# Performance work log

Hardware: AMD Instinct MI355X
Metric: run time of the kernel (lower is better)

The kernel has to match this reference:

```python
import jax, jax.numpy as jnp
import numpy as np

HEADS = 16
DIM_HEAD = 64
EPS = 1e-5


def _layernorm(x, w, b):
    mu = jnp.mean(x, axis=-1, keepdims=True)
    var = jnp.var(x, axis=-1, keepdims=True)
    return (x - mu) * jax.lax.rsqrt(var + EPS) * w + b


def setup_inputs() -> dict:
    key = jax.random.key(0)
    ks = jax.random.split(key, 6)
    B, F, Q, D = 8, 4096, 64, 1024
    inner = HEADS * DIM_HEAD  # 1024
    s = 0.02
    return {
        "features": jax.random.normal(ks[0], (B, F, D), jnp.float32),
        "latents": jax.random.normal(ks[1], (B, Q, D), jnp.float32),
        "lnm_w": jnp.ones((D,), jnp.float32),
        "lnm_b": jnp.zeros((D,), jnp.float32),
        "lnl_w": jnp.ones((D,), jnp.float32),
        "lnl_b": jnp.zeros((D,), jnp.float32),
        "Wq": jax.random.normal(ks[2], (D, inner), jnp.float32) * s,
        "Wk": jax.random.normal(ks[3], (D, inner), jnp.float32) * s,
        "Wv": jax.random.normal(ks[4], (D, inner), jnp.float32) * s,
        "Wo": jax.random.normal(ks[5], (inner, D), jnp.float32) * s,
    }


def reference(features, latents, lnm_w, lnm_b, lnl_w, lnl_b, Wq, Wk, Wv, Wo):
    B, Q = latents.shape[0], latents.shape[1]
    scale = DIM_HEAD ** (-0.5)

    x = _layernorm(features, lnm_w, lnm_b)           # (B, F, D)
    lat = _layernorm(latents, lnl_w, lnl_b)          # (B, Q, D)

    q = (lat @ Wq).reshape(B, Q, HEADS, DIM_HEAD).transpose(0, 2, 1, 3)  # b h q d
    kv_in = jnp.concatenate([x, lat], axis=1)        # (B, F+Q, D)
    FL = kv_in.shape[1]
    k = (kv_in @ Wk).reshape(B, FL, HEADS, DIM_HEAD).transpose(0, 2, 1, 3)  # b h f d
    v = (kv_in @ Wv).reshape(B, FL, HEADS, DIM_HEAD).transpose(0, 2, 1, 3)  # b h f d

    sim = jnp.einsum('bhqd,bhfd->bhqf', q * scale, k)
    alphas = jax.nn.softmax(sim, axis=-1)            # amax-subtract is folded into stable softmax
    out = jnp.einsum('bhqf,bhfv->bhqv', alphas, v)
    out = out.transpose(0, 2, 1, 3).reshape(B, Q, HEADS * DIM_HEAD)
    return out @ Wo
```

## Files before the change

### kernel.cpp

```cpp
#include <hip/hip_runtime.h>


typedef float   f32x4  __attribute__((ext_vector_type(4)));
typedef short   bf16x8 __attribute__((ext_vector_type(8)));

#define MFMA_BF16 __builtin_amdgcn_mfma_f32_16x16x32_bf16

__device__ __forceinline__ unsigned short f2bf(float f) {
  unsigned u = __float_as_uint(f);
  unsigned r = (u + 0x7fffu + ((u >> 16) & 1u)) >> 16;
  return (unsigned short)r;
}

__device__ __forceinline__ void gload_lds16(const unsigned short* g, unsigned short* l) {
  __builtin_amdgcn_global_load_lds(
      (const __attribute__((address_space(1))) unsigned int*)g,
      (__attribute__((address_space(3))) unsigned int*)l, 16, 0, 0);
}

__global__ __launch_bounds__(256) void ln_kernel(
    const float* __restrict__ features, const float* __restrict__ latents,
    const float* __restrict__ lnm_w, const float* __restrict__ lnm_b,
    const float* __restrict__ lnl_w, const float* __restrict__ lnl_b,
    unsigned short* __restrict__ kv_ln, unsigned short* __restrict__ lat_ln)
{
  const int row = blockIdx.x;
  const int b  = row / 4160;
  const int fi = row - b * 4160;
  const bool is_lat = fi >= 4096;
  const float* x = is_lat ? (latents + (size_t)(b * 64 + fi - 4096) * 1024)
                          : (features + (size_t)(b * 4096 + fi) * 1024);
  const float* wp = is_lat ? lnl_w : lnm_w;
  const float* bp = is_lat ? lnl_b : lnm_b;
  const int tid = threadIdx.x;

  float4 v = *(const float4*)(x + tid * 4);
  float s  = v.x + v.y + v.z + v.w;
  float s2 = v.x * v.x + v.y * v.y + v.z * v.z + v.w * v.w;
#pragma unroll
  for (int sh = 1; sh < 64; sh <<= 1) {
    s  += __shfl_xor(s,  sh, 64);
    s2 += __shfl_xor(s2, sh, 64);
  }
  __shared__ float red[8];
  if ((tid & 63) == 0) { red[tid >> 6] = s; red[4 + (tid >> 6)] = s2; }
  __syncthreads();
  s  = red[0] + red[1] + red[2] + red[3];
  s2 = red[4] + red[5] + red[6] + red[7];
  const float mu   = s * (1.0f / 1024.0f);
  const float var  = s2 * (1.0f / 1024.0f) - mu * mu;
  const float rstd = rsqrtf(var + 1e-5f);

  float4 w4 = *(const float4*)(wp + tid * 4);
  float4 b4 = *(const float4*)(bp + tid * 4);
  ushort4 o;
  o.x = f2bf((v.x - mu) * rstd * w4.x + b4.x);
  o.y = f2bf((v.y - mu) * rstd * w4.y + b4.y);
  o.z = f2bf((v.z - mu) * rstd * w4.z + b4.z);
  o.w = f2bf((v.w - mu) * rstd * w4.w + b4.w);
  *(ushort4*)(kv_ln + (size_t)row * 1024 + tid * 4) = o;
  if (is_lat)
    *(ushort4*)(lat_ln + (size_t)(b * 64 + fi - 4096) * 1024 + tid * 4) = o;
}

__global__ __launch_bounds__(256) void wcast_kernel(
    const float* __restrict__ Wq, const float* __restrict__ Wk,
    const float* __restrict__ Wv, const float* __restrict__ Wo,
    unsigned short* __restrict__ Wkv_t, unsigned short* __restrict__ Wq_t,
    unsigned short* __restrict__ Wo_t)
{
  __shared__ float tile[32][33];
  const int kt = blockIdx.x * 32, nt = blockIdx.y * 32;
  const int tx = threadIdx.x & 31, ty = threadIdx.x >> 5;

  const float* src; int nc; float scale = 1.0f;
  if (nt < 1024)      { src = Wk; nc = nt; }
  else if (nt < 2048) { src = Wv; nc = nt - 1024; }
  else if (nt < 3072) { src = Wq; nc = nt - 2048; scale = 0.125f; }
  else                { src = Wo; nc = nt - 3072; }

#pragma unroll
  for (int kk = 0; kk < 4; ++kk)
    tile[ty + kk * 8][tx] = src[(size_t)(kt + ty + kk * 8) * 1024 + nc + tx] * scale;
  __syncthreads();

#pragma unroll
  for (int nn = 0; nn < 4; ++nn) {
    const int ng = nt + ty + nn * 8;
    unsigned short* d;
    if (ng < 2048)      d = Wkv_t + (size_t)ng * 1024;
    else if (ng < 3072) d = Wq_t + (size_t)(ng - 2048) * 1024;
    else                d = Wo_t + (size_t)(ng - 3072) * 1024;
    d[kt + tx] = f2bf(tile[tx][ty + nn * 8]);
  }
}

__global__ __launch_bounds__(512, 4) void gemm256_bf16(
    const unsigned short* __restrict__ A,
    const unsigned short* __restrict__ Bt,
    unsigned short* __restrict__ Kp, unsigned short* __restrict__ Vp,
    int M, int N, int K)
{
  __shared__ __align__(16) unsigned short lds[36864];
  const int tid  = threadIdx.x;
  const int wave = tid >> 6, lane = tid & 63;
  const int lo = lane & 15, hi = lane >> 4;
  const int wr = wave >> 1, wc = wave & 1;

  const int nbn = gridDim.x;
  int flat = blockIdx.y * nbn + blockIdx.x;
  const int nwg = nbn * gridDim.y;
  flat = (flat & 7) * (nwg >> 3) + (flat >> 3);
  const int bm = flat / nbn, bn = flat - bm * nbn;

  int garA[2], gakA[2];
#pragma unroll
  for (int gi = 0; gi < 2; ++gi) {
    int off = gi * 8192 + tid * 16;
    int p = off ^ (((off >> 9) & 1) << 5);
    int s = p >> 10, q = p & 1023;
    garA[gi] = (s >> 1) * 16 + (q >> 6) + 128 * (s & 1);
    gakA[gi] = (q & 63) >> 1;
  }
  int grB, gkB;
  {
    int off = tid * 16;
    int p = off ^ (((off >> 9) & 1) << 5);
    int s = p >> 10, q = p & 1023;
    grB = (s >> 1) * 16 + (q >> 6) + 64 * (s & 1);
    gkB = (q & 63) >> 1;
  }
  const unsigned short* pA0 = A  + (size_t)(bm * 256 + garA[0]) * K + gakA[0];
  const unsigned short* pA1 = A  + (size_t)(bm * 256 + garA[1]) * K + gakA[1];
  const unsigned short* pB  = Bt + (size_t)(bn * 128 + grB)     * K + gkB;

  f32x4 acc[4][4];
#pragma unroll
  for (int i = 0; i < 4; ++i)
#pragma unroll
    for (int j = 0; j < 4; ++j) acc[i][j] = (f32x4){0.f, 0.f, 0.f, 0.f};

  const int NT = K >> 5;

#pragma unroll
  for (int tt = 0; tt < 2; ++tt) {
    unsigned short* bb = lds + tt * 12288;
    gload_lds16(pA0 + tt * 32, bb + wave * 512);
    gload_lds16(pA1 + tt * 32, bb + 4096 + wave * 512);
    gload_lds16(pB  + tt * 32, bb + 8192 + wave * 512);
  }
  asm volatile("s_waitcnt vmcnt(3)" ::: "memory");
  asm volatile("s_barrier" ::: "memory");

  const int swz = (lo * 32 + hi * 8) ^ ((lo & 8) << 1);
  int aAddr[4], bAddr[4];
#pragma unroll
  for (int m = 0; m < 4; ++m)
    aAddr[m] = ((((wr & 1) * 4 + m) * 2) + (wr >> 1)) * 512 + swz;
#pragma unroll
  for (int n = 0; n < 4; ++n)
    bAddr[n] = 8192 + (n * 2 + wc) * 512 + swz;

  int cur = 0;
  for (int t = 0; t < NT; ++t) {
    const unsigned short* bp = lds + cur * 12288;
    bf16x8 af[4], bf[4];
#pragma unroll
    for (int m = 0; m < 4; ++m) af[m] = *(const bf16x8*)(bp + aAddr[m]);
#pragma unroll
    for (int n = 0; n < 4; ++n) bf[n] = *(const bf16x8*)(bp + bAddr[n]);

    if (t + 2 < NT) {
      int s2 = cur + 2; if (s2 >= 3) s2 -= 3;
      unsigned short* db = lds + s2 * 12288;
      const int koff = (t + 2) * 32;
      gload_lds16(pA0 + koff, db + wave * 512);
      gload_lds16(pA1 + koff, db + 4096 + wave * 512);
      gload_lds16(pB  + koff, db + 8192 + wave * 512);
    }

    __builtin_amdgcn_s_setprio(1);
#pragma unroll
    for (int m = 0; m < 4; ++m)
#pragma unroll
      for (int n = 0; n < 4; ++n)
        acc[m][n] = MFMA_BF16(af[m], bf[n], acc[m][n], 0, 0, 0);
    __builtin_amdgcn_s_setprio(0);

    if (t + 2 < NT)      { asm volatile("s_waitcnt vmcnt(3)" ::: "memory"); }
    else if (t + 1 < NT) { asm volatile("s_waitcnt vmcnt(0)" ::: "memory"); }
    asm volatile("s_barrier" ::: "memory");
    cur = (cur == 2) ? 0 : cur + 1;
  }

#pragma unroll
  for (int m = 0; m < 4; ++m) {
    const int grow0 = bm * 256 + wr * 64 + m * 16 + hi * 4;
#pragma unroll
    for (int n = 0; n < 4; ++n) {
      const int gcol = bn * 128 + wc * 64 + n * 16 + lo;
      unsigned short* plane = (gcol & 1024) ? Vp : Kp;
      const size_t pbase = (size_t)((gcol >> 6) & 15) * 2129920 + (gcol & 63);
#pragma unroll
      for (int r = 0; r < 4; ++r)
        plane[pbase + (size_t)(grow0 + r) * 64] = f2bf(acc[m][n][r]);
    }
  }
}

template <typename CT>
__global__ __launch_bounds__(256) void gemm_tn(
    const unsigned short* __restrict__ A,
    const unsigned short* __restrict__ Bt,
    CT* __restrict__ C, int M, int N, int K)
{
  __shared__ __align__(16) unsigned short sA[2][128 * 32];
  __shared__ __align__(16) unsigned short sB[2][128 * 32];
  const int tid  = threadIdx.x;
  const int wave = tid >> 6, lane = tid & 63;
  const int bm = blockIdx.y, bn = blockIdx.x;
  const int wr = wave >> 1, wc = wave & 1;
  const int lo = lane & 15, hi = lane >> 4;
  const int srow = lane >> 2, squad = lane & 3;

  const unsigned short* gA = A  + (size_t)(bm * 128 + srow) * K + squad * 8;
  const unsigned short* gB = Bt + (size_t)(bn * 128 + srow) * K + squad * 8;

  f32x4 acc[4][4];
#pragma unroll
  for (int i = 0; i < 4; ++i)
#pragma unroll
    for (int j = 0; j < 4; ++j) acc[i][j] = (f32x4){0.f, 0.f, 0.f, 0.f};

  const int kt = K >> 5;
#pragma unroll
  for (int c = 0; c < 2; ++c) {
    const int chunk = wave * 2 + c;
    gload_lds16(gA + (size_t)chunk * 16 * K, &sA[0][chunk * 512]);
    gload_lds16(gB + (size_t)chunk * 16 * K, &sB[0][chunk * 512]);
  }
  __syncthreads();

  int buf = 0;
  for (int t = 0; t < kt; ++t) {
    if (t + 1 < kt) {
      const int k0 = (t + 1) << 5;
#pragma unroll
      for (int c = 0; c < 2; ++c) {
        const int chunk = wave * 2 + c;
        gload_lds16(gA + (size_t)chunk * 16 * K + k0, &sA[buf ^ 1][chunk * 512]);
        gload_lds16(gB + (size_t)chunk * 16 * K + k0, &sB[buf ^ 1][chunk * 512]);
      }
    }
    bf16x8 af[4], bfr[4];
#pragma unroll
    for (int i = 0; i < 4; ++i) {
      af[i]  = *(const bf16x8*)&sA[buf][(wr * 64 + i * 16 + lo) * 32 + hi * 8];
      bfr[i] = *(const bf16x8*)&sB[buf][(wc * 64 + i * 16 + lo) * 32 + hi * 8];
    }
#pragma unroll
    for (int i = 0; i < 4; ++i)
#pragma unroll
      for (int j = 0; j < 4; ++j)
        acc[i][j] = MFMA_BF16(af[i], bfr[j], acc[i][j], 0, 0, 0);
    __syncthreads();
    buf ^= 1;
  }

#pragma unroll
  for (int i = 0; i < 4; ++i) {
    const int row0 = bm * 128 + wr * 64 + i * 16 + hi * 4;
#pragma unroll
    for (int j = 0; j < 4; ++j) {
      const int col = bn * 128 + wc * 64 + j * 16 + lo;
#pragma unroll
      for (int r = 0; r < 4; ++r) {
        const size_t idx = (size_t)(row0 + r) * N + col;
        if constexpr (sizeof(CT) == 2) C[idx] = (CT)f2bf(acc[i][j][r]);
        else                            C[idx] = acc[i][j][r];
      }
    }
  }
}

__global__ __launch_bounds__(256) void attn_kernel(
    const unsigned short* __restrict__ qws,
    const unsigned short* __restrict__ Kp, const unsigned short* __restrict__ Vp,
    float* __restrict__ pacc, float* __restrict__ pml)
{
  const int bhs = blockIdx.x;
  const int s = bhs & 7, h = (bhs >> 3) & 15, b = bhs >> 7;
  const int t0 = (s * 65) >> 3;
  const int t1 = ((s + 1) * 65) >> 3;
  const int tid = threadIdx.x;
  const int wave = tid >> 6, lane = tid & 63;
  const int lo = lane & 15, hi = lane >> 4;

  __shared__ __align__(16) unsigned short sK [64][72];
  __shared__ __align__(16) unsigned short sVT[64][72];
  __shared__ __align__(16) unsigned short sP [4][16][72];

  bf16x8 qf[2];
  {
    const unsigned short* p = qws + (size_t)(b * 64 + wave * 16 + lo) * 1024 + h * 64 + hi * 8;
    qf[0] = *(const bf16x8*)p;
    qf[1] = *(const bf16x8*)(p + 32);
  }
  float m[4] = {-1e30f, -1e30f, -1e30f, -1e30f};
  float l[4] = {0.f, 0.f, 0.f, 0.f};
  f32x4 acc[4];
#pragma unroll
  for (int i = 0; i < 4; ++i) acc[i] = (f32x4){0.f, 0.f, 0.f, 0.f};

  const int frow = tid >> 2, c4 = tid & 3;
  const size_t hbase = (size_t)h * 2129920;

  bf16x8 kreg[2], vreg[2];
  {
    const size_t rb = hbase + (size_t)(b * 4160 + t0 * 64 + frow) * 64;
#pragma unroll
    for (int rr = 0; rr < 2; ++rr) {
      const int d0 = rr * 32 + c4 * 8;
      kreg[rr] = *(const bf16x8*)(Kp + rb + d0);
      vreg[rr] = *(const bf16x8*)(Vp + rb + d0);
    }
  }

  for (int t = t0; t < t1; ++t) {
    __syncthreads();
#pragma unroll
    for (int rr = 0; rr < 2; ++rr) {
      const int d0 = rr * 32 + c4 * 8;
      *(bf16x8*)&sK[frow][d0] = kreg[rr];
#pragma unroll
      for (int j = 0; j < 8; ++j) sVT[d0 + j][frow] = (unsigned short)vreg[rr][j];
    }
    __syncthreads();
    if (t + 1 < t1) {
      const size_t rb = hbase + (size_t)(b * 4160 + (t + 1) * 64 + frow) * 64;
#pragma unroll
      for (int rr = 0; rr < 2; ++rr) {
        const int d0 = rr * 32 + c4 * 8;
        kreg[rr] = *(const bf16x8*)(Kp + rb + d0);
        vreg[rr] = *(const bf16x8*)(Vp + rb + d0);
      }
    }

    f32x4 sim[4];
#pragma unroll
    for (int nf = 0; nf < 4; ++nf) {
      f32x4 a0 = (f32x4){0.f, 0.f, 0.f, 0.f};
#pragma unroll
      for (int ks = 0; ks < 2; ++ks) {
        bf16x8 kf = *(const bf16x8*)&sK[nf * 16 + lo][ks * 32 + hi * 8];
        a0 = MFMA_BF16(qf[ks], kf, a0, 0, 0, 0);
      }
      sim[nf] = a0;
    }

    float pr[4][4];
    float corr[4];
#pragma unroll
    for (int r = 0; r < 4; ++r) {
      float tm = fmaxf(fmaxf(sim[0][r], sim[1][r]), fmaxf(sim[2][r], sim[3][r]));
#pragma unroll
      for (int sh = 1; sh < 16; sh <<= 1) tm = fmaxf(tm, __shfl_xor(tm, sh, 64));
      const float mn = fmaxf(m[r], tm);
      corr[r] = __expf(m[r] - mn);
      float rs = 0.f;
#pragma unroll
      for (int nf = 0; nf < 4; ++nf) {
        float p = __expf(sim[nf][r] - mn);
        pr[r][nf] = p;
        rs += p;
      }
#pragma unroll
      for (int sh = 1; sh < 16; sh <<= 1) rs += __shfl_xor(rs, sh, 64);
      l[r] = l[r] * corr[r] + rs;
      m[r] = mn;
    }

    {
      const int r2 = lane & 3;
      float csel = r2 == 0 ? corr[0] : r2 == 1 ? corr[1] : r2 == 2 ? corr[2] : corr[3];
      const int src = ((lane & 15) >> 2) * 16 + (lane & 3);
      const float cacc = __shfl(csel, src, 64);
#pragma unroll
      for (int i = 0; i < 4; ++i) acc[i] *= cacc;
    }

#pragma unroll
    for (int r = 0; r < 4; ++r)
#pragma unroll
      for (int nf = 0; nf < 4; ++nf)
        sP[wave][hi * 4 + r][nf * 16 + lo] = f2bf(pr[r][nf]);

#pragma unroll
    for (int ks = 0; ks < 2; ++ks) {
      bf16x8 pf = *(const bf16x8*)&sP[wave][lo][ks * 32 + hi * 8];
#pragma unroll
      for (int i = 0; i < 4; ++i) {
        bf16x8 vf = *(const bf16x8*)&sVT[i * 16 + lo][ks * 32 + hi * 8];
        acc[i] = MFMA_BF16(vf, pf, acc[i], 0, 0, 0);
      }
    }
  }

  if (lo == 0) {
#pragma unroll
    for (int r = 0; r < 4; ++r) {
      pml[bhs * 128 + wave * 16 + hi * 4 + r]      = m[r];
      pml[bhs * 128 + 64 + wave * 16 + hi * 4 + r] = l[r];
    }
  }
#pragma unroll
  for (int i = 0; i < 4; ++i)
#pragma unroll
    for (int r = 0; r < 4; ++r)
      pacc[bhs * 4096 + (i * 16 + hi * 4 + r) * 64 + wave * 16 + lo] = acc[i][r];
}

__global__ __launch_bounds__(256) void attn_combine(
    const float* __restrict__ pacc, const float* __restrict__ pml,
    unsigned short* __restrict__ attn_out)
{
  const int bh = blockIdx.x;
  const int b = bh >> 4, h = bh & 15;
  const int t = threadIdx.x;
  const int q = t & 63, dg = t >> 6;
  const int base = bh << 3;

  float mm[8], ll[8];
#pragma unroll
  for (int s = 0; s < 8; ++s) {
    mm[s] = pml[(base + s) * 128 + q];
    ll[s] = pml[(base + s) * 128 + 64 + q];
  }
  float M = mm[0];
#pragma unroll
  for (int s = 1; s < 8; ++s) M = fmaxf(M, mm[s]);
  float e[8];
  float L = 0.f;
#pragma unroll
  for (int s = 0; s < 8; ++s) { e[s] = __expf(mm[s] - M); L += e[s] * ll[s]; }
  const float inv = 1.0f / L;

#pragma unroll
  for (int dd = 0; dd < 16; ++dd) {
    const int d = dg * 16 + dd;
    float v = 0.f;
#pragma unroll
    for (int s = 0; s < 8; ++s)
      v += e[s] * pacc[(base + s) * 4096 + d * 64 + q];
    attn_out[(size_t)(b * 64 + q) * 1024 + h * 64 + d] = f2bf(v * inv);
  }
}

extern "C" void kernel_launch(void* const* d_in, const int* in_sizes, int n_in,
                              void* d_out, int out_size, void* d_ws, size_t ws_size,
                              hipStream_t stream) {
  const float* features = (const float*)d_in[0];
  const float* latents  = (const float*)d_in[1];
  const float* lnm_w = (const float*)d_in[2];
  const float* lnm_b = (const float*)d_in[3];
  const float* lnl_w = (const float*)d_in[4];
  const float* lnl_b = (const float*)d_in[5];
  const float* Wq = (const float*)d_in[6];
  const float* Wk = (const float*)d_in[7];
  const float* Wv = (const float*)d_in[8];
  const float* Wo = (const float*)d_in[9];
  float* out = (float*)d_out;

  char* ws = (char*)d_ws;
  unsigned short* kv_ln    = (unsigned short*)(ws);
  unsigned short* Wkv_t    = (unsigned short*)(ws + 68157440);
  unsigned short* Wq_t     = (unsigned short*)(ws + 72351744);
  unsigned short* Wo_t     = (unsigned short*)(ws + 74448896);
  unsigned short* lat_ln   = (unsigned short*)(ws + 76546048);
  unsigned short* q_ws     = (unsigned short*)(ws + 77594624);
  unsigned short* attn_out = (unsigned short*)(ws + 78643200);
  unsigned short* Kp       = (unsigned short*)(ws + 79691776);
  unsigned short* Vp       = (unsigned short*)(ws + 147849216);
  float* pacc = (float*)(ws);
  float* pml  = (float*)(ws + 16777216);

  ln_kernel<<<33280, 256, 0, stream>>>(features, latents, lnm_w, lnm_b, lnl_w, lnl_b,
                                       kv_ln, lat_ln);
  wcast_kernel<<<dim3(32, 128), 256, 0, stream>>>(Wq, Wk, Wv, Wo, Wkv_t, Wq_t, Wo_t);
  gemm256_bf16<<<dim3(16, 130), 512, 0, stream>>>(kv_ln, Wkv_t, Kp, Vp, 33280, 2048, 1024);
  gemm_tn<unsigned short><<<dim3(8, 4), 256, 0, stream>>>(lat_ln, Wq_t, q_ws, 512, 1024, 1024);
  attn_kernel<<<1024, 256, 0, stream>>>(q_ws, Kp, Vp, pacc, pml);
  attn_combine<<<128, 256, 0, stream>>>(pacc, pml, attn_out);
  gemm_tn<float><<<dim3(8, 4), 256, 0, stream>>>(attn_out, Wo_t, out, 512, 1024, 1024);
}
```

Before: 289.3 us.

## Store V pre-transposed from projection GEMM via LDS staging for attention

```diff
diff --git a/kernel.cpp b/kernel.cpp
--- a/kernel.cpp
+++ b/kernel.cpp
@@ -98,7 +98,7 @@
 __global__ __launch_bounds__(512, 4) void gemm256_bf16(
     const unsigned short* __restrict__ A,
     const unsigned short* __restrict__ Bt,
-    unsigned short* __restrict__ Kp, unsigned short* __restrict__ Vp,
+    unsigned short* __restrict__ Kp, unsigned short* __restrict__ Vt,
     int M, int N, int K)
 {
   __shared__ __align__(16) unsigned short lds[36864];
@@ -193,17 +193,43 @@
     cur = (cur == 2) ? 0 : cur + 1;
   }
 
-#pragma unroll
-  for (int m = 0; m < 4; ++m) {
-    const int grow0 = bm * 256 + wr * 64 + m * 16 + hi * 4;
-#pragma unroll
-    for (int n = 0; n < 4; ++n) {
-      const int gcol = bn * 128 + wc * 64 + n * 16 + lo;
-      unsigned short* plane = (gcol & 1024) ? Vp : Kp;
-      const size_t pbase = (size_t)((gcol >> 6) & 15) * 2129920 + (gcol & 63);
-#pragma unroll
-      for (int r = 0; r < 4; ++r)
-        plane[pbase + (size_t)(grow0 + r) * 64] = f2bf(acc[m][n][r]);
+  if (bn < 8) {
+#pragma unroll
+    for (int m = 0; m < 4; ++m) {
+      const int grow0 = bm * 256 + wr * 64 + m * 16 + hi * 4;
+#pragma unroll
+      for (int n = 0; n < 4; ++n) {
+        const int gcol = bn * 128 + wc * 64 + n * 16 + lo;
+        const size_t pbase = (size_t)(gcol >> 6) * 2129920 + (gcol & 63);
+#pragma unroll
+        for (int r = 0; r < 4; ++r)
+          Kp[pbase + (size_t)(grow0 + r) * 64] = f2bf(acc[m][n][r]);
+      }
+    }
+  } else {
+    __syncthreads();
+    unsigned short* ldsT = lds;
+#pragma unroll
+    for (int m = 0; m < 4; ++m) {
+      const int row_l = wr * 64 + m * 16 + hi * 4;
+#pragma unroll
+      for (int n = 0; n < 4; ++n) {
+        const int col_l = wc * 64 + n * 16 + lo;
+#pragma unroll
+        for (int r = 0; r < 4; ++r)
+          ldsT[col_l * 264 + row_l + r] = f2bf(acc[m][n][r]);
+      }
+    }
+    __syncthreads();
+#pragma unroll
+    for (int it = 0; it < 8; ++it) {
+      const int col_l = it * 16 + (tid >> 5);
+      const int rl = (tid & 31) * 8;
+      bf16x8 v = *(const bf16x8*)&ldsT[col_l * 264 + rl];
+      const int hcol = (bn - 8) * 128 + col_l;
+      const size_t dst = (size_t)(hcol >> 6) * 2129920
+                       + (size_t)(hcol & 63) * 33280 + bm * 256 + rl;
+      *(bf16x8*)&Vt[dst] = v;
     }
   }
 }
@@ -285,7 +311,7 @@
 
 __global__ __launch_bounds__(256) void attn_kernel(
     const unsigned short* __restrict__ qws,
-    const unsigned short* __restrict__ Kp, const unsigned short* __restrict__ Vp,
+    const unsigned short* __restrict__ Kp, const unsigned short* __restrict__ Vt,
     float* __restrict__ pacc, float* __restrict__ pml)
 {
   const int bhs = blockIdx.x;
@@ -313,37 +339,37 @@
   for (int i = 0; i < 4; ++i) acc[i] = (f32x4){0.f, 0.f, 0.f, 0.f};
 
   const int frow = tid >> 2, c4 = tid & 3;
+  const int vd = tid >> 3, vfo = (tid & 7) * 8;
   const size_t hbase = (size_t)h * 2129920;
 
   bf16x8 kreg[2], vreg[2];
   {
-    const size_t rb = hbase + (size_t)(b * 4160 + t0 * 64 + frow) * 64;
-#pragma unroll
-    for (int rr = 0; rr < 2; ++rr) {
-      const int d0 = rr * 32 + c4 * 8;
-      kreg[rr] = *(const bf16x8*)(Kp + rb + d0);
-      vreg[rr] = *(const bf16x8*)(Vp + rb + d0);
-    }
+    const size_t rowb = (size_t)(b * 4160 + t0 * 64);
+#pragma unroll
+    for (int rr = 0; rr < 2; ++rr)
+      kreg[rr] = *(const bf16x8*)(Kp + hbase + (rowb + frow) * 64 + rr * 32 + c4 * 8);
+#pragma unroll
+    for (int p = 0; p < 2; ++p)
+      vreg[p] = *(const bf16x8*)(Vt + hbase + (size_t)(vd + p * 32) * 33280 + rowb + vfo);
   }
 
   for (int t = t0; t < t1; ++t) {
     __syncthreads();
 #pragma unroll
-    for (int rr = 0; rr < 2; ++rr) {
-      const int d0 = rr * 32 + c4 * 8;
-      *(bf16x8*)&sK[frow][d0] = kreg[rr];
-#pragma unroll
-      for (int j = 0; j < 8; ++j) sVT[d0 + j][frow] = (unsigned short)vreg[rr][j];
-    }
+    for (int rr = 0; rr < 2; ++rr)
+      *(bf16x8*)&sK[frow][rr * 32 + c4 * 8] = kreg[rr];
+#pragma unroll
+    for (int p = 0; p < 2; ++p)
+      *(bf16x8*)&sVT[vd + p * 32][vfo] = vreg[p];
     __syncthreads();
     if (t + 1 < t1) {
-      const size_t rb = hbase + (size_t)(b * 4160 + (t + 1) * 64 + frow) * 64;
-#pragma unroll
-      for (int rr = 0; rr < 2; ++rr) {
-        const int d0 = rr * 32 + c4 * 8;
-        kreg[rr] = *(const bf16x8*)(Kp + rb + d0);
-        vreg[rr] = *(const bf16x8*)(Vp + rb + d0);
-      }
+      const size_t rowb = (size_t)(b * 4160 + (t + 1) * 64);
+#pragma unroll
+      for (int rr = 0; rr < 2; ++rr)
+        kreg[rr] = *(const bf16x8*)(Kp + hbase + (rowb + frow) * 64 + rr * 32 + c4 * 8);
+#pragma unroll
+      for (int p = 0; p < 2; ++p)
+        vreg[p] = *(const bf16x8*)(Vt + hbase + (size_t)(vd + p * 32) * 33280 + rowb + vfo);
     }
 
     f32x4 sim[4];
@@ -480,16 +506,16 @@
   unsigned short* q_ws     = (unsigned short*)(ws + 77594624);
   unsigned short* attn_out = (unsigned short*)(ws + 78643200);
   unsigned short* Kp       = (unsigned short*)(ws + 79691776);
-  unsigned short* Vp       = (unsigned short*)(ws + 147849216);
+  unsigned short* Vt       = (unsigned short*)(ws + 147849216);
   float* pacc = (float*)(ws);
   float* pml  = (float*)(ws + 16777216);
 
   ln_kernel<<<33280, 256, 0, stream>>>(features, latents, lnm_w, lnm_b, lnl_w, lnl_b,
                                        kv_ln, lat_ln);
   wcast_kernel<<<dim3(32, 128), 256, 0, stream>>>(Wq, Wk, Wv, Wo, Wkv_t, Wq_t, Wo_t);
-  gemm256_bf16<<<dim3(16, 130), 512, 0, stream>>>(kv_ln, Wkv_t, Kp, Vp, 33280, 2048, 1024);
+  gemm256_bf16<<<dim3(16, 130), 512, 0, stream>>>(kv_ln, Wkv_t, Kp, Vt, 33280, 2048, 1024);
   gemm_tn<unsigned short><<<dim3(8, 4), 256, 0, stream>>>(lat_ln, Wq_t, q_ws, 512, 1024, 1024);
-  attn_kernel<<<1024, 256, 0, stream>>>(q_ws, Kp, Vp, pacc, pml);
+  attn_kernel<<<1024, 256, 0, stream>>>(q_ws, Kp, Vt, pacc, pml);
   attn_combine<<<128, 256, 0, stream>>>(pacc, pml, attn_out);
   gemm_tn<float><<<dim3(8, 4), 256, 0, stream>>>(attn_out, Wo_t, out, 512, 1024, 1024);
 }
```

Result: no change. 285.1 us (-1.5%).
